# Performance work log

Measured on AMD Instinct MI355X. Metric: run time of the kernel, lower is better.

## Reference

```python
import jax, jax.numpy as jnp
import numpy as np

B, S, H = 2, 2048, 1024
NH = 16
HD = H // NH


def setup_inputs() -> dict:
    key = jax.random.key(0)
    ks = jax.random.split(key, 9)
    std = 1.0 / np.sqrt(H)
    inp = {"x": jax.random.normal(ks[0], (B, S, H), dtype=jnp.float32)}
    names = ["Wq", "Wk", "Wv", "Wo"]
    for i, n in enumerate(names):
        inp[n] = jax.random.uniform(ks[1 + i], (H, H), dtype=jnp.float32, minval=-std, maxval=std)
        inp["b" + n[1:]] = jax.random.uniform(ks[5 + i], (H,), dtype=jnp.float32, minval=-std, maxval=std)
    return inp


def reference(x, Wq, Wk, Wv, Wo, bq, bk, bv, bo):
    scale = HD ** -0.5
    # projections: torch Linear is x @ W.T + b
    def proj(W, b):
        y = jnp.einsum('bsh,oh->bso', x, W) + b
        return y.reshape(B, S, NH, HD).transpose(0, 2, 1, 3)  # [B, NH, S, HD]
    Q = proj(Wq, bq)
    K = proj(Wk, bk)
    V = proj(Wv, bv)
    scores = jnp.einsum('bhqd,bhkd->bhqk', Q, K) * scale  # [B, NH, S, S]
    attn = jax.nn.softmax(scores, axis=-1)
    ctx = jnp.einsum('bhqk,bhkd->bhqd', attn, V)
    ctx = ctx.transpose(0, 2, 1, 3).reshape(B, S, H)
    out = jnp.einsum('bsh,oh->bso', ctx, Wo) + bo
    avg_attention = attn.mean(axis=1).mean(axis=1)  # [B, S] (mean over heads, then query dim)
    return out, avg_attention
```

## Files before the change

### kernel.cpp

```cpp
#include <hip/hip_runtime.h>
#include <hip/hip_bf16.h>

#define B_  2
#define S_  2048
#define H_  1024
#define NH_ 16
#define HD_ 64
#define NTOK (B_*S_)

typedef __attribute__((ext_vector_type(8))) short bf16x8;
typedef __attribute__((ext_vector_type(4))) float f32x4;

#define SC2 0.18033688011112042f
#define AVGINV (1.f/((float)NH_*(float)S_))

static __device__ __forceinline__ ushort f2bf(float f) {
    __hip_bfloat16 h = __float2bfloat16(f);
    return *reinterpret_cast<ushort*>(&h);
}
static __device__ __forceinline__ uint cvt_pk_bf16(float lo, float hi) {
    uint r;
    asm("v_cvt_pk_bf16_f32 %0, %1, %2" : "=v"(r) : "v"(lo), "v"(hi));
    return r;
}

static __device__ __forceinline__ void gload_lds16(const void* g, void* l) {
    __builtin_amdgcn_global_load_lds(
        (const __attribute__((address_space(1))) void*)g,
        (__attribute__((address_space(3))) void*)l,
        16, 0, 0);
}

struct PrepArgs {
    const float* src[5];
    ushort*      dst[5];
    float*       zero;
};

static __device__ __forceinline__ void conv8(const float* __restrict__ s,
                                             ushort* __restrict__ d, int i)
{
    const float4 a = reinterpret_cast<const float4*>(s)[2*i + 0];
    const float4 b = reinterpret_cast<const float4*>(s)[2*i + 1];
    ushort u[8];
    u[0] = f2bf(a.x); u[1] = f2bf(a.y); u[2] = f2bf(a.z); u[3] = f2bf(a.w);
    u[4] = f2bf(b.x); u[5] = f2bf(b.y); u[6] = f2bf(b.z); u[7] = f2bf(b.w);
    reinterpret_cast<uint4*>(d)[i] = *reinterpret_cast<uint4*>(u);
}

__global__ __launch_bounds__(256) void prep(PrepArgs a)
{
    int bid = blockIdx.x;
    const int t = threadIdx.x;
    if (bid < 2048) {
        conv8(a.src[0], a.dst[0], bid*256 + t);
        return;
    }
    bid -= 2048;
    if (bid < 2048) {
        const int wi = 1 + (bid >> 9);
        const int i  = (bid & 511)*256 + t;
        conv8(a.src[wi], a.dst[wi], i);
        return;
    }
    bid -= 2048;
    const int i = bid*256 + t;
    if (i < NTOK) a.zero[i] = 0.f;
}

__global__ __launch_bounds__(256) void transpose_v(
    const ushort* __restrict__ Vb, ushort* __restrict__ Vt)
{
    __shared__ ushort T[64][72];
    const int t  = threadIdx.x;
    const int b  = blockIdx.z;
    const int h  = blockIdx.y;
    const int s0 = blockIdx.x * 64;
    const int r  = t >> 2;
    const int c0 = (t & 3) * 16;

    const ushort* src = Vb + (size_t)(b*S_ + s0 + r)*H_ + h*HD_ + c0;
    *reinterpret_cast<uint4*>(&T[r][c0])     = *reinterpret_cast<const uint4*>(src);
    *reinterpret_cast<uint4*>(&T[r][c0 + 8]) = *reinterpret_cast<const uint4*>(src + 8);
    __syncthreads();

    const int d = r;
    ushort tmp[16];
#pragma unroll
    for (int k = 0; k < 16; ++k) tmp[k] = T[c0 + k][d];
    ushort* dst = Vt + ((size_t)((b*NH_ + h)*HD_ + d))*S_ + s0 + c0;
    *reinterpret_cast<uint4*>(dst)     = *reinterpret_cast<uint4*>(&tmp[0]);
    *reinterpret_cast<uint4*>(dst + 8) = *reinterpret_cast<uint4*>(&tmp[8]);
}

struct GemmArgs {
    const ushort* W[3];
    const float*  bias[3];
    void*         Y[3];
    float         scale[3];
};

__global__ __launch_bounds__(256) void gemm_qkv(
    const ushort* __restrict__ A, GemmArgs args, int M, int N, int K)
{
    constexpr int MREP = 4;
    constexpr int BM = MREP * 32;
    __shared__ __align__(16) ushort As[BM * 64];
    __shared__ __align__(16) ushort Bs[128 * 64];

    const int z = blockIdx.z;
    const ushort* __restrict__ W   = args.W[z];
    const float*  __restrict__ bia = args.bias[z];
    const float sc = args.scale[z];

    const int t  = threadIdx.x;
    const int w  = t >> 6;
    const int l  = t & 63;
    const int lq = l >> 4;
    const int ln = l & 15;
    const int wr = w >> 1;
    const int wc = w & 1;
    const int m0 = blockIdx.x * BM;
    const int n0 = blockIdx.y * 128;
    const int srow = l >> 3;
    const int scol = (l & 7) * 8;

    f32x4 acc[MREP][4];
#pragma unroll
    for (int m = 0; m < MREP; ++m)
#pragma unroll
        for (int n = 0; n < 4; ++n) acc[m][n] = f32x4{0.f, 0.f, 0.f, 0.f};

    for (int k0 = 0; k0 < K; k0 += 64) {
        __syncthreads();
#pragma unroll
        for (int i = 0; i < BM/32; ++i) {
            const int rb = i*32 + w*8;
            gload_lds16(A + (size_t)(m0 + rb + srow)*K + k0 + scol, &As[rb*64]);
        }
#pragma unroll
        for (int i = 0; i < 4; ++i) {
            const int rb = i*32 + w*8;
            gload_lds16(W + (size_t)(n0 + rb + srow)*K + k0 + scol, &Bs[rb*64]);
        }
        __syncthreads();
#pragma unroll
        for (int ks = 0; ks < 2; ++ks) {
            bf16x8 bfr[4];
#pragma unroll
            for (int n = 0; n < 4; ++n)
                bfr[n] = *reinterpret_cast<const bf16x8*>(&Bs[(wc*64 + n*16 + ln)*64 + ks*32 + lq*8]);
#pragma unroll
            for (int m = 0; m < MREP; ++m) {
                const bf16x8 afr = *reinterpret_cast<const bf16x8*>(&As[(wr*MREP*16 + m*16 + ln)*64 + ks*32 + lq*8]);
#pragma unroll
                for (int n = 0; n < 4; ++n)
                    acc[m][n] = __builtin_amdgcn_mfma_f32_16x16x32_bf16(afr, bfr[n], acc[m][n], 0, 0, 0);
            }
        }
    }

    float bv[4];
#pragma unroll
    for (int n = 0; n < 4; ++n) bv[n] = bia[n0 + wc*64 + n*16 + ln];

    ushort* Y = (ushort*)args.Y[z];
#pragma unroll
    for (int m = 0; m < MREP; ++m) {
#pragma unroll
        for (int r = 0; r < 4; ++r) {
            const size_t row = (size_t)(m0 + wr*MREP*16 + m*16 + lq*4 + r);
#pragma unroll
            for (int n = 0; n < 4; ++n) {
                const int col = n0 + wc*64 + n*16 + ln;
                Y[row*N + col] = f2bf((acc[m][n][r] + bv[n]) * sc);
            }
        }
    }
}

__global__ __launch_bounds__(256) void attn_pv(
    const ushort* __restrict__ Qb, const ushort* __restrict__ Kb,
    const ushort* __restrict__ Vtg, ushort* __restrict__ ctx,
    float* __restrict__ il2_g)
{
    __shared__ __align__(16) ushort Ks0[64*64];
    __shared__ __align__(16) ushort Ks1[64*64];
    __shared__ __align__(16) ushort Vs0[64*64];
    __shared__ __align__(16) ushort Vs1[64*64];
    __shared__ __align__(16) ushort Ps[4][16*64];

    const int id = blockIdx.x;
    const int qt_ = (id >> 3) & 31;
    const int bh  = (id & 7) + ((id >> 8) << 3);
    const int b   = bh >> 4;
    const int h   = bh & 15;
    const int q0  = qt_ * 64;

    const int t  = threadIdx.x;
    const int w  = t >> 6;
    const int l  = t & 63;
    const int lq = l >> 4;
    const int ln = l & 15;
    const int ln7 = ln & 7;

    bf16x8 qf[2];
    {
        const ushort* qrow = Qb + ((size_t)(b*S_ + q0 + w*16 + ln))*H_ + h*HD_ + lq*8;
        qf[0] = *reinterpret_cast<const bf16x8*>(qrow);
        qf[1] = *reinterpret_cast<const bf16x8*>(qrow + 32);
    }

    bf16x8 onesb;
#pragma unroll
    for (int j = 0; j < 8; ++j) onesb[j] = (short)0x3F80;

    const f32x4 ZED = f32x4{0.f, 0.f, 0.f, 0.f};

    size_t koff[2], voff[2];
    int    dsto[2];
#pragma unroll
    for (int i = 0; i < 2; ++i) {
        const int chunk = i*256 + t;
        const int row   = chunk >> 3;
        const int c8    = (chunk & 7) ^ (row & 7);
        koff[i] = (size_t)(b*S_ + row)*H_ + h*HD_ + c8*8;
        voff[i] = ((size_t)((b*NH_ + h)*HD_ + row))*S_ + c8*8;
        dsto[i] = chunk*8;
    }

    f32x4 lsacc = ZED;
    f32x4 oacc[4];
#pragma unroll
    for (int nt = 0; nt < 4; ++nt) oacc[nt] = ZED;

    auto tile_body = [&](const ushort* __restrict__ ksb, const ushort* __restrict__ vsb,
                         int pre_kt, bool do_pre,
                         ushort* __restrict__ kdst, ushort* __restrict__ vdst) {
        if (do_pre) {
#pragma unroll
            for (int i = 0; i < 2; ++i) {
                gload_lds16(Kb + koff[i] + (size_t)pre_kt*H_, &kdst[dsto[i]]);
                gload_lds16(Vtg + voff[i] + pre_kt, &vdst[dsto[i]]);
            }
        }

        f32x4 sacc[4];
        {
            bf16x8 kb[4];
#pragma unroll
            for (int nt = 0; nt < 4; ++nt)
                kb[nt] = *reinterpret_cast<const bf16x8*>(
                    &ksb[(nt*16 + ln)*64 + ((lq ^ ln7) * 8)]);
#pragma unroll
            for (int nt = 0; nt < 4; ++nt)
                sacc[nt] = __builtin_amdgcn_mfma_f32_16x16x32_bf16(
                    kb[nt], qf[0], ZED, 0, 0, 0);
        }
        {
            bf16x8 kb[4];
#pragma unroll
            for (int nt = 0; nt < 4; ++nt)
                kb[nt] = *reinterpret_cast<const bf16x8*>(
                    &ksb[(nt*16 + ln)*64 + (((4 + lq) ^ ln7) * 8)]);
#pragma unroll
            for (int nt = 0; nt < 4; ++nt)
                sacc[nt] = __builtin_amdgcn_mfma_f32_16x16x32_bf16(
                    kb[nt], qf[1], sacc[nt], 0, 0, 0);
        }

#pragma unroll
        for (int nt = 0; nt < 4; ++nt) {
            const float e0 = exp2f(sacc[nt][0]);
            const float e1 = exp2f(sacc[nt][1]);
            const float e2 = exp2f(sacc[nt][2]);
            const float e3 = exp2f(sacc[nt][3]);
            uint2 pk;
            pk.x = cvt_pk_bf16(e0, e1);
            pk.y = cvt_pk_bf16(e2, e3);
            const int wch = (nt*2 + (lq >> 1)) ^ ln7;
            *reinterpret_cast<uint2*>(&Ps[w][ln*64 + wch*8 + (lq & 1)*4]) = pk;
        }

#pragma unroll
        for (int ks = 0; ks < 2; ++ks) {
            const bf16x8 pa = *reinterpret_cast<const bf16x8*>(
                &Ps[w][ln*64 + (((ks*4 + lq) ^ ln7) * 8)]);
            lsacc = __builtin_amdgcn_mfma_f32_16x16x32_bf16(pa, onesb, lsacc, 0, 0, 0);
#pragma unroll
            for (int nt = 0; nt < 4; ++nt) {
                const bf16x8 vb8 = *reinterpret_cast<const bf16x8*>(
                    &vsb[(nt*16 + ln)*64 + (((ks*4 + lq) ^ ln7) * 8)]);
                oacc[nt] = __builtin_amdgcn_mfma_f32_16x16x32_bf16(
                    pa, vb8, oacc[nt], 0, 0, 0);
            }
        }

        __syncthreads();
    };

#pragma unroll
    for (int i = 0; i < 2; ++i) {
        gload_lds16(Kb + koff[i], &Ks0[dsto[i]]);
        gload_lds16(Vtg + voff[i], &Vs0[dsto[i]]);
    }
    __syncthreads();

    for (int kt = 0; kt < S_; kt += 128) {
        tile_body(Ks0, Vs0, kt + 64, true, Ks1, Vs1);
        tile_body(Ks1, Vs1, kt + 128, kt + 128 < S_, Ks0, Vs0);
    }

    float ivr[4];
#pragma unroll
    for (int r = 0; r < 4; ++r) ivr[r] = 1.f / lsacc[r];

    if (ln == 0) {
        float4 o;
        o.x = -__log2f(lsacc[0]);
        o.y = -__log2f(lsacc[1]);
        o.z = -__log2f(lsacc[2]);
        o.w = -__log2f(lsacc[3]);
        *reinterpret_cast<float4*>(
            il2_g + (size_t)(b*NH_ + h)*S_ + q0 + w*16 + lq*4) = o;
    }

    ushort* crow = ctx + ((size_t)(b*S_ + q0 + w*16 + lq*4))*H_ + h*HD_ + ln;
#pragma unroll
    for (int r = 0; r < 4; ++r)
#pragma unroll
        for (int nt = 0; nt < 4; ++nt)
            crow[(size_t)r*H_ + nt*16] = f2bf(oacc[nt][r] * ivr[r]);
}

struct FusedArgs {
    const ushort* Qb; const ushort* Kb;
    const float*  il2; float* avg_out;
    const ushort* A;  const ushort* W;
    const float*  bias; float* Y;
};

__global__ __launch_bounds__(256) void colsum_outproj(FusedArgs fa)
{
    __shared__ __align__(16) char smem[32768];
    const int id = blockIdx.x;
    const int t  = threadIdx.x;
    const int w  = t >> 6;
    const int l  = t & 63;
    const int lq = l >> 4;
    const int ln = l & 15;
    const int ln7 = ln & 7;
    const f32x4 ZED = f32x4{0.f, 0.f, 0.f, 0.f};

    if (id < 1024) {
        ushort* KsT = (ushort*)smem;
        ushort* Qs0 = (ushort*)(smem + 8192);
        ushort* Qs1 = (ushort*)(smem + 16384);
        float*  iv  = (float*)(smem + 24576);

        const int kt_ = (id >> 3) & 31;
        const int bh  = (id & 7) + ((id >> 8) << 3);
        const int b   = bh >> 4;
        const int h   = bh & 15;
        const int k0  = kt_ * 64;

        int crow_[2], cc8[2], dsto[2];
#pragma unroll
        for (int i = 0; i < 2; ++i) {
            const int chunk = i*256 + t;
            crow_[i] = chunk >> 3;
            cc8[i]   = (chunk & 7) ^ (crow_[i] & 7);
            dsto[i]  = chunk*8;
        }

#pragma unroll
        for (int i = 0; i < 2; ++i) {
            gload_lds16(fa.Kb + (size_t)(b*S_ + k0 + crow_[i])*H_ + h*HD_ + cc8[i]*8, &KsT[dsto[i]]);
            gload_lds16(fa.il2 + (size_t)bh*S_ + (i*256 + t)*4, &iv[(i*256 + t)*4]);
            gload_lds16(fa.Qb + (size_t)(b*S_ + crow_[i])*H_ + h*HD_ + cc8[i]*8, &Qs0[dsto[i]]);
        }
        __syncthreads();

        bf16x8 kf[2];
#pragma unroll
        for (int ks = 0; ks < 2; ++ks)
            kf[ks] = *reinterpret_cast<const bf16x8*>(
                &KsT[(w*16 + ln)*64 + (((ks*4 + lq) ^ ln7) * 8)]);

        float cs4[4] = {0.f, 0.f, 0.f, 0.f};

        for (int qt = 0; qt < S_; qt += 128) {
#pragma unroll
            for (int i = 0; i < 2; ++i)
                gload_lds16(fa.Qb + (size_t)(b*S_ + qt + 64 + crow_[i])*H_ + h*HD_ + cc8[i]*8,
                            &Qs1[dsto[i]]);
#pragma unroll
            for (int c = 0; c < 4; ++c) {
                const bf16x8 a0 = *reinterpret_cast<const bf16x8*>(
                    &Qs0[(c*16 + ln)*64 + ((lq ^ ln7) * 8)]);
                const bf16x8 a1 = *reinterpret_cast<const bf16x8*>(
                    &Qs0[(c*16 + ln)*64 + (((4 + lq) ^ ln7) * 8)]);
                f32x4 sacc = __builtin_amdgcn_mfma_f32_16x16x32_bf16(a0, kf[0], ZED, 0, 0, 0);
                sacc = __builtin_amdgcn_mfma_f32_16x16x32_bf16(a1, kf[1], sacc, 0, 0, 0);
                const f32x4 iv4 = *reinterpret_cast<const f32x4*>(&iv[qt + c*16 + lq*4]);
#pragma unroll
                for (int r = 0; r < 4; ++r)
                    cs4[r] += exp2f(sacc[r] + iv4[r]);
            }
            __syncthreads();

            if (qt + 128 < S_) {
#pragma unroll
                for (int i = 0; i < 2; ++i)
                    gload_lds16(fa.Qb + (size_t)(b*S_ + qt + 128 + crow_[i])*H_ + h*HD_ + cc8[i]*8,
                                &Qs0[dsto[i]]);
            }
#pragma unroll
            for (int c = 0; c < 4; ++c) {
                const bf16x8 a0 = *reinterpret_cast<const bf16x8*>(
                    &Qs1[(c*16 + ln)*64 + ((lq ^ ln7) * 8)]);
                const bf16x8 a1 = *reinterpret_cast<const bf16x8*>(
                    &Qs1[(c*16 + ln)*64 + (((4 + lq) ^ ln7) * 8)]);
                f32x4 sacc = __builtin_amdgcn_mfma_f32_16x16x32_bf16(a0, kf[0], ZED, 0, 0, 0);
                sacc = __builtin_amdgcn_mfma_f32_16x16x32_bf16(a1, kf[1], sacc, 0, 0, 0);
                const f32x4 iv4 = *reinterpret_cast<const f32x4*>(&iv[qt + 64 + c*16 + lq*4]);
#pragma unroll
                for (int r = 0; r < 4; ++r)
                    cs4[r] += exp2f(sacc[r] + iv4[r]);
            }
            __syncthreads();
        }

        float cs = (cs4[0] + cs4[1]) + (cs4[2] + cs4[3]);
        cs += __shfl_xor(cs, 16);
        cs += __shfl_xor(cs, 32);
        if (l < 16)
            atomicAdd(&fa.avg_out[(size_t)b*S_ + k0 + w*16 + l], cs * AVGINV);
    } else {
        ushort* As = (ushort*)smem;
        ushort* Bs = (ushort*)(smem + 8192);

        const int g  = id - 1024;
        const int m0 = (g & 63) * 64;
        const int n0 = (g >> 6) * 128;
        const int wr = w >> 1;
        const int wc = w & 1;
        const int srow = l >> 3;
        const int scol = (l & 7) * 8;

        f32x4 acc[2][4];
#pragma unroll
        for (int m = 0; m < 2; ++m)
#pragma unroll
            for (int n = 0; n < 4; ++n) acc[m][n] = ZED;

        for (int k0 = 0; k0 < H_; k0 += 64) {
            __syncthreads();
#pragma unroll
            for (int i = 0; i < 2; ++i) {
                const int rb = i*32 + w*8;
                gload_lds16(fa.A + (size_t)(m0 + rb + srow)*H_ + k0 + scol, &As[rb*64]);
            }
#pragma unroll
            for (int i = 0; i < 4; ++i) {
                const int rb = i*32 + w*8;
                gload_lds16(fa.W + (size_t)(n0 + rb + srow)*H_ + k0 + scol, &Bs[rb*64]);
            }
            __syncthreads();
#pragma unroll
            for (int ks = 0; ks < 2; ++ks) {
                bf16x8 bfr[4];
#pragma unroll
                for (int n = 0; n < 4; ++n)
                    bfr[n] = *reinterpret_cast<const bf16x8*>(&Bs[(wc*64 + n*16 + ln)*64 + ks*32 + lq*8]);
#pragma unroll
                for (int m = 0; m < 2; ++m) {
                    const bf16x8 afr = *reinterpret_cast<const bf16x8*>(&As[(wr*32 + m*16 + ln)*64 + ks*32 + lq*8]);
#pragma unroll
                    for (int n = 0; n < 4; ++n)
                        acc[m][n] = __builtin_amdgcn_mfma_f32_16x16x32_bf16(afr, bfr[n], acc[m][n], 0, 0, 0);
                }
            }
        }

        float bv[4];
#pragma unroll
        for (int n = 0; n < 4; ++n) bv[n] = fa.bias[n0 + wc*64 + n*16 + ln];

#pragma unroll
        for (int m = 0; m < 2; ++m) {
#pragma unroll
            for (int r = 0; r < 4; ++r) {
                const size_t row = (size_t)(m0 + wr*32 + m*16 + lq*4 + r);
#pragma unroll
                for (int n = 0; n < 4; ++n) {
                    const int col = n0 + wc*64 + n*16 + ln;
                    fa.Y[row*H_ + col] = acc[m][n][r] + bv[n];
                }
            }
        }
    }
}

extern "C" void kernel_launch(void* const* d_in, const int* in_sizes, int n_in,
                              void* d_out, int out_size, void* d_ws, size_t ws_size,
                              hipStream_t stream)
{
    const float* x  = (const float*)d_in[0];
    const float* Wq = (const float*)d_in[1];
    const float* bq = (const float*)d_in[2];
    const float* Wk = (const float*)d_in[3];
    const float* bk = (const float*)d_in[4];
    const float* Wv = (const float*)d_in[5];
    const float* bv = (const float*)d_in[6];
    const float* Wo = (const float*)d_in[7];
    const float* bo = (const float*)d_in[8];

    float* out     = (float*)d_out;
    float* avg_out = out + (size_t)NTOK * H_;

    char* ws = (char*)d_ws;
    const size_t mat  = (size_t)NTOK * H_ * sizeof(ushort);
    const size_t wmat = (size_t)H_ * H_ * sizeof(ushort);
    ushort* xb   = (ushort*)(ws);
    ushort* Qb   = (ushort*)(ws + mat);
    ushort* Kb   = (ushort*)(ws + 2*mat);
    ushort* Vb   = (ushort*)(ws + 3*mat);
    ushort* Vtg  = (ushort*)(ws + 4*mat);
    ushort* Wqb  = (ushort*)(ws + 5*mat);
    ushort* Wkb  = (ushort*)(ws + 5*mat + wmat);
    ushort* Wvb  = (ushort*)(ws + 5*mat + 2*wmat);
    ushort* Wob  = (ushort*)(ws + 5*mat + 3*wmat);
    float*  il2  = (float*)(ws + 5*mat + 4*wmat);
    ushort* ctxb = xb;

    const dim3 blk(256);

    {
        PrepArgs pa;
        pa.src[0] = x;  pa.dst[0] = xb;
        pa.src[1] = Wq; pa.dst[1] = Wqb;
        pa.src[2] = Wk; pa.dst[2] = Wkb;
        pa.src[3] = Wv; pa.dst[3] = Wvb;
        pa.src[4] = Wo; pa.dst[4] = Wob;
        pa.zero = avg_out;
        prep<<<dim3(4112), blk, 0, stream>>>(pa);
    }

    {
        GemmArgs ga;
        ga.W[0] = Wqb; ga.W[1] = Wkb; ga.W[2] = Wvb;
        ga.bias[0] = bq; ga.bias[1] = bk; ga.bias[2] = bv;
        ga.Y[0] = Qb; ga.Y[1] = Kb; ga.Y[2] = Vb;
        ga.scale[0] = SC2; ga.scale[1] = 1.f; ga.scale[2] = 1.f;
        gemm_qkv<<<dim3(NTOK/128, H_/128, 3), blk, 0, stream>>>(xb, ga, NTOK, H_, H_);
    }

    transpose_v<<<dim3(S_/64, NH_, B_), blk, 0, stream>>>(Vb, Vtg);

    attn_pv<<<dim3(1024), blk, 0, stream>>>(Qb, Kb, Vtg, ctxb, il2);

    {
        FusedArgs fa;
        fa.Qb = Qb; fa.Kb = Kb; fa.il2 = il2; fa.avg_out = avg_out;
        fa.A = ctxb; fa.W = Wob; fa.bias = bo; fa.Y = out;
        colsum_outproj<<<dim3(1536), blk, 0, stream>>>(fa);
    }
}
```

Measured before the change: 180.5 us.

## Process 128 query rows per attention block to reuse K/V tiles

Each attention block now covers 128 query rows instead of 64, with every wave handling two 16-row query slices that share the same K and V fragments read from LDS. This halves the global K/V traffic and LDS fragment loads per query row and halves the grid to 512 blocks. In exchange it doubles accumulator registers and the P scratch in shared memory, adds a launch-bounds occupancy hint, and leaves fewer blocks to spread across the CUs.

```diff
diff --git a/kernel.cpp b/kernel.cpp
--- a/kernel.cpp
+++ b/kernel.cpp
@@ -179,7 +179,7 @@
     }
 }
 
-__global__ __launch_bounds__(256) void attn_pv(
+__global__ __launch_bounds__(256, 2) void attn_pv(
     const ushort* __restrict__ Qb, const ushort* __restrict__ Kb,
     const ushort* __restrict__ Vtg, ushort* __restrict__ ctx,
     float* __restrict__ il2_g)
@@ -188,14 +188,14 @@
     __shared__ __align__(16) ushort Ks1[64*64];
     __shared__ __align__(16) ushort Vs0[64*64];
     __shared__ __align__(16) ushort Vs1[64*64];
-    __shared__ __align__(16) ushort Ps[4][16*64];
-
-    const int id = blockIdx.x;
-    const int qt_ = (id >> 3) & 31;
-    const int bh  = (id & 7) + ((id >> 8) << 3);
+    __shared__ __align__(16) ushort Ps[4][32*64];
+
+    const int id  = blockIdx.x;
+    const int qt_ = (id >> 3) & 15;
+    const int bh  = (id & 7) + ((id >> 7) << 3);
     const int b   = bh >> 4;
     const int h   = bh & 15;
-    const int q0  = qt_ * 64;
+    const int q0  = qt_ * 128;
 
     const int t  = threadIdx.x;
     const int w  = t >> 6;
@@ -204,11 +204,12 @@
     const int ln = l & 15;
     const int ln7 = ln & 7;
 
-    bf16x8 qf[2];
-    {
-        const ushort* qrow = Qb + ((size_t)(b*S_ + q0 + w*16 + ln))*H_ + h*HD_ + lq*8;
-        qf[0] = *reinterpret_cast<const bf16x8*>(qrow);
-        qf[1] = *reinterpret_cast<const bf16x8*>(qrow + 32);
+    bf16x8 qf[2][2];
+#pragma unroll
+    for (int qs = 0; qs < 2; ++qs) {
+        const ushort* qrow = Qb + ((size_t)(b*S_ + q0 + w*32 + qs*16 + ln))*H_ + h*HD_ + lq*8;
+        qf[qs][0] = *reinterpret_cast<const bf16x8*>(qrow);
+        qf[qs][1] = *reinterpret_cast<const bf16x8*>(qrow + 32);
     }
 
     bf16x8 onesb;
@@ -229,10 +230,12 @@
         dsto[i] = chunk*8;
     }
 
-    f32x4 lsacc = ZED;
-    f32x4 oacc[4];
-#pragma unroll
-    for (int nt = 0; nt < 4; ++nt) oacc[nt] = ZED;
+    f32x4 lsacc[2] = {ZED, ZED};
+    f32x4 oacc[2][4];
+#pragma unroll
+    for (int qs = 0; qs < 2; ++qs)
+#pragma unroll
+        for (int nt = 0; nt < 4; ++nt) oacc[qs][nt] = ZED;
 
     auto tile_body = [&](const ushort* __restrict__ ksb, const ushort* __restrict__ vsb,
                          int pre_kt, bool do_pre,
@@ -245,7 +248,7 @@
             }
         }
 
-        f32x4 sacc[4];
+        f32x4 sacc[2][4];
         {
             bf16x8 kb[4];
 #pragma unroll
@@ -253,9 +256,11 @@
                 kb[nt] = *reinterpret_cast<const bf16x8*>(
                     &ksb[(nt*16 + ln)*64 + ((lq ^ ln7) * 8)]);
 #pragma unroll
-            for (int nt = 0; nt < 4; ++nt)
-                sacc[nt] = __builtin_amdgcn_mfma_f32_16x16x32_bf16(
-                    kb[nt], qf[0], ZED, 0, 0, 0);
+            for (int qs = 0; qs < 2; ++qs)
+#pragma unroll
+                for (int nt = 0; nt < 4; ++nt)
+                    sacc[qs][nt] = __builtin_amdgcn_mfma_f32_16x16x32_bf16(
+                        kb[nt], qf[qs][0], ZED, 0, 0, 0);
         }
         {
             bf16x8 kb[4];
@@ -264,35 +269,48 @@
                 kb[nt] = *reinterpret_cast<const bf16x8*>(
                     &ksb[(nt*16 + ln)*64 + (((4 + lq) ^ ln7) * 8)]);
 #pragma unroll
-            for (int nt = 0; nt < 4; ++nt)
-                sacc[nt] = __builtin_amdgcn_mfma_f32_16x16x32_bf16(
-                    kb[nt], qf[1], sacc[nt], 0, 0, 0);
-        }
-
-#pragma unroll
-        for (int nt = 0; nt < 4; ++nt) {
-            const float e0 = exp2f(sacc[nt][0]);
-            const float e1 = exp2f(sacc[nt][1]);
-            const float e2 = exp2f(sacc[nt][2]);
-            const float e3 = exp2f(sacc[nt][3]);
-            uint2 pk;
-            pk.x = cvt_pk_bf16(e0, e1);
-            pk.y = cvt_pk_bf16(e2, e3);
-            const int wch = (nt*2 + (lq >> 1)) ^ ln7;
-            *reinterpret_cast<uint2*>(&Ps[w][ln*64 + wch*8 + (lq & 1)*4]) = pk;
+            for (int qs = 0; qs < 2; ++qs)
+#pragma unroll
+                for (int nt = 0; nt < 4; ++nt)
+                    sacc[qs][nt] = __builtin_amdgcn_mfma_f32_16x16x32_bf16(
+                        kb[nt], qf[qs][1], sacc[qs][nt], 0, 0, 0);
+        }
+
+#pragma unroll
+        for (int qs = 0; qs < 2; ++qs) {
+#pragma unroll
+            for (int nt = 0; nt < 4; ++nt) {
+                const float e0 = exp2f(sacc[qs][nt][0]);
+                const float e1 = exp2f(sacc[qs][nt][1]);
+                const float e2 = exp2f(sacc[qs][nt][2]);
+                const float e3 = exp2f(sacc[qs][nt][3]);
+                uint2 pk;
+                pk.x = cvt_pk_bf16(e0, e1);
+                pk.y = cvt_pk_bf16(e2, e3);
+                const int wch = (nt*2 + (lq >> 1)) ^ ln7;
+                *reinterpret_cast<uint2*>(
+                    &Ps[w][(qs*16 + ln)*64 + wch*8 + (lq & 1)*4]) = pk;
+            }
         }
 
 #pragma unroll
         for (int ks = 0; ks < 2; ++ks) {
-            const bf16x8 pa = *reinterpret_cast<const bf16x8*>(
-                &Ps[w][ln*64 + (((ks*4 + lq) ^ ln7) * 8)]);
-            lsacc = __builtin_amdgcn_mfma_f32_16x16x32_bf16(pa, onesb, lsacc, 0, 0, 0);
+            bf16x8 pa[2];
+#pragma unroll
+            for (int qs = 0; qs < 2; ++qs) {
+                pa[qs] = *reinterpret_cast<const bf16x8*>(
+                    &Ps[w][(qs*16 + ln)*64 + (((ks*4 + lq) ^ ln7) * 8)]);
+                lsacc[qs] = __builtin_amdgcn_mfma_f32_16x16x32_bf16(
+                    pa[qs], onesb, lsacc[qs], 0, 0, 0);
+            }
 #pragma unroll
             for (int nt = 0; nt < 4; ++nt) {
                 const bf16x8 vb8 = *reinterpret_cast<const bf16x8*>(
                     &vsb[(nt*16 + ln)*64 + (((ks*4 + lq) ^ ln7) * 8)]);
-                oacc[nt] = __builtin_amdgcn_mfma_f32_16x16x32_bf16(
-                    pa, vb8, oacc[nt], 0, 0, 0);
+#pragma unroll
+                for (int qs = 0; qs < 2; ++qs)
+                    oacc[qs][nt] = __builtin_amdgcn_mfma_f32_16x16x32_bf16(
+                        pa[qs], vb8, oacc[qs][nt], 0, 0, 0);
             }
         }
 
@@ -311,26 +329,29 @@
         tile_body(Ks1, Vs1, kt + 128, kt + 128 < S_, Ks0, Vs0);
     }
 
-    float ivr[4];
-#pragma unroll
-    for (int r = 0; r < 4; ++r) ivr[r] = 1.f / lsacc[r];
-
-    if (ln == 0) {
-        float4 o;
-        o.x = -__log2f(lsacc[0]);
-        o.y = -__log2f(lsacc[1]);
-        o.z = -__log2f(lsacc[2]);
-        o.w = -__log2f(lsacc[3]);
-        *reinterpret_cast<float4*>(
-            il2_g + (size_t)(b*NH_ + h)*S_ + q0 + w*16 + lq*4) = o;
-    }
-
-    ushort* crow = ctx + ((size_t)(b*S_ + q0 + w*16 + lq*4))*H_ + h*HD_ + ln;
-#pragma unroll
-    for (int r = 0; r < 4; ++r)
-#pragma unroll
-        for (int nt = 0; nt < 4; ++nt)
-            crow[(size_t)r*H_ + nt*16] = f2bf(oacc[nt][r] * ivr[r]);
+#pragma unroll
+    for (int qs = 0; qs < 2; ++qs) {
+        float ivr[4];
+#pragma unroll
+        for (int r = 0; r < 4; ++r) ivr[r] = 1.f / lsacc[qs][r];
+
+        if (ln == 0) {
+            float4 o;
+            o.x = -__log2f(lsacc[qs][0]);
+            o.y = -__log2f(lsacc[qs][1]);
+            o.z = -__log2f(lsacc[qs][2]);
+            o.w = -__log2f(lsacc[qs][3]);
+            *reinterpret_cast<float4*>(
+                il2_g + (size_t)(b*NH_ + h)*S_ + q0 + w*32 + qs*16 + lq*4) = o;
+        }
+
+        ushort* crow = ctx + ((size_t)(b*S_ + q0 + w*32 + qs*16 + lq*4))*H_ + h*HD_ + ln;
+#pragma unroll
+        for (int r = 0; r < 4; ++r)
+#pragma unroll
+            for (int nt = 0; nt < 4; ++nt)
+                crow[(size_t)r*H_ + nt*16] = f2bf(oacc[qs][nt][r] * ivr[r]);
+    }
 }
 
 struct FusedArgs {
@@ -558,7 +579,7 @@
 
     transpose_v<<<dim3(S_/64, NH_, B_), blk, 0, stream>>>(Vb, Vtg);
 
-    attn_pv<<<dim3(1024), blk, 0, stream>>>(Qb, Kb, Vtg, ctxb, il2);
+    attn_pv<<<dim3(512), blk, 0, stream>>>(Qb, Kb, Vtg, ctxb, il2);
 
     {
         FusedArgs fa;
```

Result: faster. 170.8 us (-5.3%).

## Switch attention kernel to 32x32x16 MFMA with register-resident P via permlane swap

Applied to the files above, without the earlier changes.

Rewrites the attention-PV kernel so each wave handles 32 query rows using 32x32x16 bf16 MFMAs instead of 16x16x32. The probability tile is no longer staged through shared memory; it is repacked in registers with v_permlane32_swap so the S accumulator layout matches the A-operand layout of the PV MFMA. Blocks now cover 128 queries, which halves the grid to 512 and doubles K/V tile reuse per block. The cost is higher accumulator register pressure, possibly lower occupancy, and narrower scalar ctx stores.

```diff
diff --git a/kernel.cpp b/kernel.cpp
--- a/kernel.cpp
+++ b/kernel.cpp
@@ -8,8 +8,9 @@
 #define HD_ 64
 #define NTOK (B_*S_)
 
-typedef __attribute__((ext_vector_type(8))) short bf16x8;
-typedef __attribute__((ext_vector_type(4))) float f32x4;
+typedef __attribute__((ext_vector_type(8)))  short bf16x8;
+typedef __attribute__((ext_vector_type(4)))  float f32x4;
+typedef __attribute__((ext_vector_type(16))) float f32x16;
 
 #define SC2 0.18033688011112042f
 #define AVGINV (1.f/((float)NH_*(float)S_))
@@ -188,34 +189,35 @@
     __shared__ __align__(16) ushort Ks1[64*64];
     __shared__ __align__(16) ushort Vs0[64*64];
     __shared__ __align__(16) ushort Vs1[64*64];
-    __shared__ __align__(16) ushort Ps[4][16*64];
-
-    const int id = blockIdx.x;
-    const int qt_ = (id >> 3) & 31;
-    const int bh  = (id & 7) + ((id >> 8) << 3);
+
+    const int id  = blockIdx.x;
+    const int qt_ = (id >> 3) & 15;
+    const int bh  = (id & 7) + ((id >> 7) << 3);
     const int b   = bh >> 4;
     const int h   = bh & 15;
-    const int q0  = qt_ * 64;
+    const int q0  = qt_ * 128;
 
     const int t  = threadIdx.x;
     const int w  = t >> 6;
     const int l  = t & 63;
-    const int lq = l >> 4;
-    const int ln = l & 15;
-    const int ln7 = ln & 7;
-
-    bf16x8 qf[2];
+    const int c  = l & 31;
+    const int hi = l >> 5;
+    const int c7 = c & 7;
+
+    bf16x8 qf[4];
     {
-        const ushort* qrow = Qb + ((size_t)(b*S_ + q0 + w*16 + ln))*H_ + h*HD_ + lq*8;
-        qf[0] = *reinterpret_cast<const bf16x8*>(qrow);
-        qf[1] = *reinterpret_cast<const bf16x8*>(qrow + 32);
+        const ushort* qrow = Qb + ((size_t)(b*S_ + q0 + w*32 + c))*H_ + h*HD_ + hi*8;
+#pragma unroll
+        for (int s = 0; s < 4; ++s)
+            qf[s] = *reinterpret_cast<const bf16x8*>(qrow + s*16);
     }
 
     bf16x8 onesb;
 #pragma unroll
     for (int j = 0; j < 8; ++j) onesb[j] = (short)0x3F80;
 
-    const f32x4 ZED = f32x4{0.f, 0.f, 0.f, 0.f};
+    f32x16 lsacc = {};
+    f32x16 oacc[2] = {{}, {}};
 
     size_t koff[2], voff[2];
     int    dsto[2];
@@ -229,11 +231,6 @@
         dsto[i] = chunk*8;
     }
 
-    f32x4 lsacc = ZED;
-    f32x4 oacc[4];
-#pragma unroll
-    for (int nt = 0; nt < 4; ++nt) oacc[nt] = ZED;
-
     auto tile_body = [&](const ushort* __restrict__ ksb, const ushort* __restrict__ vsb,
                          int pre_kt, bool do_pre,
                          ushort* __restrict__ kdst, ushort* __restrict__ vdst) {
@@ -245,54 +242,46 @@
             }
         }
 
-        f32x4 sacc[4];
-        {
-            bf16x8 kb[4];
-#pragma unroll
-            for (int nt = 0; nt < 4; ++nt)
-                kb[nt] = *reinterpret_cast<const bf16x8*>(
-                    &ksb[(nt*16 + ln)*64 + ((lq ^ ln7) * 8)]);
-#pragma unroll
-            for (int nt = 0; nt < 4; ++nt)
-                sacc[nt] = __builtin_amdgcn_mfma_f32_16x16x32_bf16(
-                    kb[nt], qf[0], ZED, 0, 0, 0);
-        }
-        {
-            bf16x8 kb[4];
-#pragma unroll
-            for (int nt = 0; nt < 4; ++nt)
-                kb[nt] = *reinterpret_cast<const bf16x8*>(
-                    &ksb[(nt*16 + ln)*64 + (((4 + lq) ^ ln7) * 8)]);
-#pragma unroll
-            for (int nt = 0; nt < 4; ++nt)
-                sacc[nt] = __builtin_amdgcn_mfma_f32_16x16x32_bf16(
-                    kb[nt], qf[1], sacc[nt], 0, 0, 0);
-        }
-
-#pragma unroll
-        for (int nt = 0; nt < 4; ++nt) {
-            const float e0 = exp2f(sacc[nt][0]);
-            const float e1 = exp2f(sacc[nt][1]);
-            const float e2 = exp2f(sacc[nt][2]);
-            const float e3 = exp2f(sacc[nt][3]);
-            uint2 pk;
-            pk.x = cvt_pk_bf16(e0, e1);
-            pk.y = cvt_pk_bf16(e2, e3);
-            const int wch = (nt*2 + (lq >> 1)) ^ ln7;
-            *reinterpret_cast<uint2*>(&Ps[w][ln*64 + wch*8 + (lq & 1)*4]) = pk;
-        }
-
-#pragma unroll
-        for (int ks = 0; ks < 2; ++ks) {
-            const bf16x8 pa = *reinterpret_cast<const bf16x8*>(
-                &Ps[w][ln*64 + (((ks*4 + lq) ^ ln7) * 8)]);
-            lsacc = __builtin_amdgcn_mfma_f32_16x16x32_bf16(pa, onesb, lsacc, 0, 0, 0);
-#pragma unroll
-            for (int nt = 0; nt < 4; ++nt) {
-                const bf16x8 vb8 = *reinterpret_cast<const bf16x8*>(
-                    &vsb[(nt*16 + ln)*64 + (((ks*4 + lq) ^ ln7) * 8)]);
-                oacc[nt] = __builtin_amdgcn_mfma_f32_16x16x32_bf16(
-                    pa, vb8, oacc[nt], 0, 0, 0);
+#pragma unroll
+        for (int sub = 0; sub < 2; ++sub) {
+            f32x16 sacc;
+            {
+                const bf16x8 kb = *reinterpret_cast<const bf16x8*>(
+                    &ksb[(sub*32 + c)*64 + ((hi ^ c7) * 8)]);
+                f32x16 zed = {};
+                sacc = __builtin_amdgcn_mfma_f32_32x32x16_bf16(kb, qf[0], zed, 0, 0, 0);
+            }
+#pragma unroll
+            for (int s = 1; s < 4; ++s) {
+                const bf16x8 kb = *reinterpret_cast<const bf16x8*>(
+                    &ksb[(sub*32 + c)*64 + (((s*2 + hi) ^ c7) * 8)]);
+                sacc = __builtin_amdgcn_mfma_f32_32x32x16_bf16(kb, qf[s], sacc, 0, 0, 0);
+            }
+
+            float e[16];
+#pragma unroll
+            for (int r = 0; r < 16; ++r) e[r] = exp2f(sacc[r]);
+
+#pragma unroll
+            for (int win = 0; win < 2; ++win) {
+                const int e0 = win*8;
+                uint x = cvt_pk_bf16(e[e0+0], e[e0+1]);
+                uint y = cvt_pk_bf16(e[e0+2], e[e0+3]);
+                uint z = cvt_pk_bf16(e[e0+4], e[e0+5]);
+                uint wv = cvt_pk_bf16(e[e0+6], e[e0+7]);
+                asm("v_permlane32_swap_b32 %0, %1" : "+v"(x), "+v"(z));
+                asm("v_permlane32_swap_b32 %0, %1" : "+v"(y), "+v"(wv));
+                uint pau[4] = {x, y, z, wv};
+                const bf16x8 pa = *reinterpret_cast<const bf16x8*>(pau);
+
+                lsacc = __builtin_amdgcn_mfma_f32_32x32x16_bf16(pa, onesb, lsacc, 0, 0, 0);
+
+#pragma unroll
+                for (int dsub = 0; dsub < 2; ++dsub) {
+                    const bf16x8 vb = *reinterpret_cast<const bf16x8*>(
+                        &vsb[(dsub*32 + c)*64 + (((sub*4 + win*2 + hi) ^ c7) * 8)]);
+                    oacc[dsub] = __builtin_amdgcn_mfma_f32_32x32x16_bf16(pa, vb, oacc[dsub], 0, 0, 0);
+                }
             }
         }
 
@@ -311,26 +300,22 @@
         tile_body(Ks1, Vs1, kt + 128, kt + 128 < S_, Ks0, Vs0);
     }
 
-    float ivr[4];
-#pragma unroll
-    for (int r = 0; r < 4; ++r) ivr[r] = 1.f / lsacc[r];
-
-    if (ln == 0) {
-        float4 o;
-        o.x = -__log2f(lsacc[0]);
-        o.y = -__log2f(lsacc[1]);
-        o.z = -__log2f(lsacc[2]);
-        o.w = -__log2f(lsacc[3]);
-        *reinterpret_cast<float4*>(
-            il2_g + (size_t)(b*NH_ + h)*S_ + q0 + w*16 + lq*4) = o;
-    }
-
-    ushort* crow = ctx + ((size_t)(b*S_ + q0 + w*16 + lq*4))*H_ + h*HD_ + ln;
-#pragma unroll
-    for (int r = 0; r < 4; ++r)
-#pragma unroll
-        for (int nt = 0; nt < 4; ++nt)
-            crow[(size_t)r*H_ + nt*16] = f2bf(oacc[nt][r] * ivr[r]);
+    if (c == 0) {
+#pragma unroll
+        for (int r = 0; r < 16; ++r) {
+            const int qrow = (r & 3) + 8*(r >> 2) + 4*hi;
+            il2_g[(size_t)(b*NH_ + h)*S_ + q0 + w*32 + qrow] = -__log2f(lsacc[r]);
+        }
+    }
+
+#pragma unroll
+    for (int r = 0; r < 16; ++r) {
+        const int qrow = (r & 3) + 8*(r >> 2) + 4*hi;
+        const float iv = 1.f / lsacc[r];
+        ushort* crow_p = ctx + ((size_t)(b*S_ + q0 + w*32 + qrow))*H_ + h*HD_ + c;
+        crow_p[0]  = f2bf(oacc[0][r] * iv);
+        crow_p[32] = f2bf(oacc[1][r] * iv);
+    }
 }
 
 struct FusedArgs {
@@ -395,14 +380,14 @@
                 gload_lds16(fa.Qb + (size_t)(b*S_ + qt + 64 + crow_[i])*H_ + h*HD_ + cc8[i]*8,
                             &Qs1[dsto[i]]);
 #pragma unroll
-            for (int c = 0; c < 4; ++c) {
+            for (int cc = 0; cc < 4; ++cc) {
                 const bf16x8 a0 = *reinterpret_cast<const bf16x8*>(
-                    &Qs0[(c*16 + ln)*64 + ((lq ^ ln7) * 8)]);
+                    &Qs0[(cc*16 + ln)*64 + ((lq ^ ln7) * 8)]);
                 const bf16x8 a1 = *reinterpret_cast<const bf16x8*>(
-                    &Qs0[(c*16 + ln)*64 + (((4 + lq) ^ ln7) * 8)]);
+                    &Qs0[(cc*16 + ln)*64 + (((4 + lq) ^ ln7) * 8)]);
                 f32x4 sacc = __builtin_amdgcn_mfma_f32_16x16x32_bf16(a0, kf[0], ZED, 0, 0, 0);
                 sacc = __builtin_amdgcn_mfma_f32_16x16x32_bf16(a1, kf[1], sacc, 0, 0, 0);
-                const f32x4 iv4 = *reinterpret_cast<const f32x4*>(&iv[qt + c*16 + lq*4]);
+                const f32x4 iv4 = *reinterpret_cast<const f32x4*>(&iv[qt + cc*16 + lq*4]);
 #pragma unroll
                 for (int r = 0; r < 4; ++r)
                     cs4[r] += exp2f(sacc[r] + iv4[r]);
@@ -416,14 +401,14 @@
                                 &Qs0[dsto[i]]);
             }
 #pragma unroll
-            for (int c = 0; c < 4; ++c) {
+            for (int cc = 0; cc < 4; ++cc) {
                 const bf16x8 a0 = *reinterpret_cast<const bf16x8*>(
-                    &Qs1[(c*16 + ln)*64 + ((lq ^ ln7) * 8)]);
+                    &Qs1[(cc*16 + ln)*64 + ((lq ^ ln7) * 8)]);
                 const bf16x8 a1 = *reinterpret_cast<const bf16x8*>(
-                    &Qs1[(c*16 + ln)*64 + (((4 + lq) ^ ln7) * 8)]);
+                    &Qs1[(cc*16 + ln)*64 + (((4 + lq) ^ ln7) * 8)]);
                 f32x4 sacc = __builtin_amdgcn_mfma_f32_16x16x32_bf16(a0, kf[0], ZED, 0, 0, 0);
                 sacc = __builtin_amdgcn_mfma_f32_16x16x32_bf16(a1, kf[1], sacc, 0, 0, 0);
-                const f32x4 iv4 = *reinterpret_cast<const f32x4*>(&iv[qt + 64 + c*16 + lq*4]);
+                const f32x4 iv4 = *reinterpret_cast<const f32x4*>(&iv[qt + 64 + cc*16 + lq*4]);
 #pragma unroll
                 for (int r = 0; r < 4; ++r)
                     cs4[r] += exp2f(sacc[r] + iv4[r]);
@@ -558,7 +543,7 @@
 
     transpose_v<<<dim3(S_/64, NH_, B_), blk, 0, stream>>>(Vb, Vtg);
 
-    attn_pv<<<dim3(1024), blk, 0, stream>>>(Qb, Kb, Vtg, ctxb, il2);
+    attn_pv<<<dim3(512), blk, 0, stream>>>(Qb, Kb, Vtg, ctxb, il2);
 
     {
         FusedArgs fa;
```

Measured after the change: 174.7 us. 3.2% less time.
